# Kernel optimization log

Hardware: AMD Instinct MI355X
Metric: run time of the kernel (lower is better)

Reference implementation:

```python
import jax, jax.numpy as jnp
import numpy as np
from jax import lax

B, CIN, LIN = 65536, 1, 274
D, S, H, NL = 16, 18, 4, 4
DH = D // H  # 4
HID = 64
EPS = 1e-5

def layer_norm(x, g, b):
    m = jnp.mean(x, axis=-1, keepdims=True)
    v = jnp.mean(jnp.square(x - m), axis=-1, keepdims=True)
    return (x - m) * lax.rsqrt(v + EPS) * g + b

def setup_inputs() -> dict:
    key = jax.random.key(0)
    ks = jax.random.split(key, 16)
    n = lambda k, shp, s=0.05: jax.random.normal(k, shp, dtype=jnp.float32) * s
    return {
        "x": jax.random.normal(ks[0], (B, CIN, LIN), dtype=jnp.float32),
        "patch_w": n(ks[1], (D, CIN, 16), 0.2),   # Conv1d weight (O,I,K)
        "patch_b": jnp.zeros((D,), jnp.float32),
        "pos_embed": n(ks[2], (1, S, D), 0.02),
        "ln1_g": jnp.ones((NL, D), jnp.float32),
        "ln1_b": jnp.zeros((NL, D), jnp.float32),
        "qkv_w": n(ks[3], (NL, 3 * D, D), 0.2),    # in_proj_weight per layer
        "qkv_b": jnp.zeros((NL, 3 * D), jnp.float32),
        "out_w": n(ks[4], (NL, D, D), 0.2),
        "out_b": jnp.zeros((NL, D), jnp.float32),
        "ln2_g": jnp.ones((NL, D), jnp.float32),
        "ln2_b": jnp.zeros((NL, D), jnp.float32),
        "mlp_w1": n(ks[5], (NL, HID, D), 0.2),
        "mlp_b1": jnp.zeros((NL, HID), jnp.float32),
        "mlp_w2": n(ks[6], (NL, D, HID), 0.2),
        "mlp_b2": jnp.zeros((NL, D), jnp.float32),
        "lnf_g": jnp.ones((D,), jnp.float32),
        "lnf_b": jnp.zeros((D,), jnp.float32),
        "dec_w": n(ks[7], (D, CIN, 16), 0.2),      # ConvTranspose1d weight (I,O,K)
        "dec_b": jnp.zeros((CIN,), jnp.float32),
    }

def reference(x, patch_w, patch_b, pos_embed, ln1_g, ln1_b, qkv_w, qkv_b,
              out_w, out_b, ln2_g, ln2_b, mlp_w1, mlp_b1, mlp_w2, mlp_b2,
              lnf_g, lnf_b, dec_w, dec_b):
    dn = ('NCH', 'OIH', 'NCH')
    # patchify: (B,1,274) -> (B,16,18) -> (B,18,16)
    h = lax.conv_general_dilated(x, patch_w, (16,), [(7, 7)], dimension_numbers=dn)
    h = h + patch_b[None, :, None]
    h = jnp.transpose(h, (0, 2, 1)) + pos_embed
    scale = 1.0 / np.sqrt(DH)
    for i in range(NL):
        xn = layer_norm(h, ln1_g[i], ln1_b[i])
        qkv = xn @ qkv_w[i].T + qkv_b[i]                      # (B,S,3D)
        q, k, v = jnp.split(qkv, 3, axis=-1)
        q = q.reshape(B, S, H, DH)
        k = k.reshape(B, S, H, DH)
        v = v.reshape(B, S, H, DH)
        att = jnp.einsum('bqhd,bkhd->bhqk', q, k) * scale
        att = jax.nn.softmax(att, axis=-1)
        o = jnp.einsum('bhqk,bkhd->bqhd', att, v).reshape(B, S, D)
        h = h + (o @ out_w[i].T + out_b[i])
        xn2 = layer_norm(h, ln2_g[i], ln2_b[i])
        m = jax.nn.gelu(xn2 @ mlp_w1[i].T + mlp_b1[i], approximate=False)
        h = h + (m @ mlp_w2[i].T + mlp_b2[i])
    h = layer_norm(h, lnf_g, lnf_b)
    z = jnp.transpose(h, (0, 2, 1))                            # (B,16,18)
    # ConvTranspose1d(k=16, s=16, p=7): lhs_dilation=16, pad=k-1-p=8, flipped kernel
    w_t = jnp.transpose(jnp.flip(dec_w, axis=-1), (1, 0, 2))   # (O=1, I=16, 16)
    out = lax.conv_general_dilated(z, w_t, (1,), [(8, 8)], lhs_dilation=(16,),
                                   dimension_numbers=dn)
    out = out + dec_b[None, :, None]                            # (B,1,274)
    return out, z
```

## Files before the change

### kernel.cpp

```cpp
#include <hip/hip_runtime.h>
#include <math.h>
#include <stdint.h>

#define NB      65536
#define LIN     274
#define SEQ     18
#define DM      16
#define NH      4
#define HID     64
#define NLAYER  4
#define EPSF    1e-5f

#define EPB      8
#define NTHREADS 192
#define SMEM_F32 3456
#define VOFF_F32 1152

typedef _Float16 h2    __attribute__((ext_vector_type(2)));
typedef _Float16 f16x4 __attribute__((ext_vector_type(4)));
typedef float    f32x4 __attribute__((ext_vector_type(4)));
typedef __fp16   hf2_raw __attribute__((ext_vector_type(2)));

#if __has_builtin(__builtin_amdgcn_fdot2)
__device__ __forceinline__ float fdot2(h2 a, h2 b, float c) { return __builtin_amdgcn_fdot2(a, b, c, false); }
#else
__device__ __forceinline__ float fdot2(h2 a, h2 b, float c) { return c + (float)a[0] * (float)b[0] + (float)a[1] * (float)b[1]; }
#endif
#if __has_builtin(__builtin_amdgcn_cvt_pkrtz)
__device__ __forceinline__ h2 pkrtz(float a, float b) {
    hf2_raw r = __builtin_amdgcn_cvt_pkrtz(a, b);
    return __builtin_bit_cast(h2, r);
}
#else
__device__ __forceinline__ h2 pkrtz(float a, float b) { h2 r; r[0] = (_Float16)a; r[1] = (_Float16)b; return r; }
#endif

#if __has_builtin(__builtin_amdgcn_mfma_f32_16x16x16f16)
__device__ __forceinline__ f32x4 MFMA16(f16x4 a, f16x4 b, f32x4 c) {
    return __builtin_amdgcn_mfma_f32_16x16x16f16(a, b, c, 0, 0, 0);
}
#elif __has_builtin(__builtin_amdgcn_mfma_f32_16x16x16_f16)
__device__ __forceinline__ f32x4 MFMA16(f16x4 a, f16x4 b, f32x4 c) {
    return __builtin_amdgcn_mfma_f32_16x16x16_f16(a, b, c, 0, 0, 0);
}
#else
__device__ __forceinline__ f32x4 MFMA16(f16x4 a, f16x4 b, f32x4 c) {
    f32x4 d;
    asm volatile("v_mfma_f32_16x16x16_f16 %0, %1, %2, %3"
                 : "=v"(d) : "v"(a), "v"(b), "v"(c));
    return d;
}
#endif

__device__ __forceinline__ float fast_rcp(float x)  { return __builtin_amdgcn_rcpf(x); }
__device__ __forceinline__ float fast_rsq(float x)  { return __builtin_amdgcn_rsqf(x); }
__device__ __forceinline__ float fast_exp2(float x) { return __builtin_amdgcn_exp2f(x); }

__device__ __forceinline__ float gelu_tanh(float t) {
    const float A = 0.79788456080286536f;
    const float B = 0.03567740814183430f;
    float t2 = t * t;
    float u  = t * fmaf(t2, B, A);
    float e  = fast_exp2(u * 2.88539008177792681f);
    float r  = fast_rcp(e + 1.0f);
    return fmaf(-t, r, t);
}

__device__ __forceinline__ f16x4 pk4(float a, float b, float c, float d) {
    h2 lo = pkrtz(a, b), hi = pkrtz(c, d);
    f16x4 r; r[0] = lo[0]; r[1] = lo[1]; r[2] = hi[0]; r[3] = hi[1];
    return r;
}
__device__ __forceinline__ f32x4 ld4(const float* p) {
    float4 t = *(const float4*)p;
    f32x4 r; r[0] = t.x; r[1] = t.y; r[2] = t.z; r[3] = t.w;
    return r;
}

#define WS_H2_COUNT 6400

__global__ __launch_bounds__(512) void prep_weights(
    const float* __restrict__ patch_w, const float* __restrict__ dec_w,
    const float* __restrict__ qkv_w, const float* __restrict__ out_w,
    const float* __restrict__ mlp_w1, const float* __restrict__ mlp_w2,
    h2* __restrict__ ws)
{
    int i = blockIdx.x * 512 + threadIdx.x;
    if (i >= WS_H2_COUNT) return;
    int tile = i >> 7;
    int lane = (i >> 1) & 63;
    int p    = i & 1;
    int row  = lane & 15;
    int kb   = (lane >> 4) * 4 + 2 * p;
    float a, b;
    if (tile == 0)      { a = patch_w[row * 16 + kb];     b = patch_w[row * 16 + kb + 1]; }
    else if (tile == 1) { a = dec_w[kb * 16 + row];       b = dec_w[(kb + 1) * 16 + row]; }
    else {
        int t2 = tile - 2, li = t2 / 12, j = t2 % 12;
        const float* s;
        if (j < 3)       s = qkv_w  + li * 768  + (j * 16 + row) * 16 + kb;
        else if (j == 3) s = out_w  + li * 256  + row * 16 + kb;
        else if (j < 8)  s = mlp_w1 + li * 1024 + ((j - 4) * 16 + row) * 16 + kb;
        else             s = mlp_w2 + li * 1024 + row * 64 + (j - 8) * 16 + kb;
        a = s[0]; b = s[1];
    }
    ws[i] = pkrtz(a, b);
}

__global__ __launch_bounds__(NTHREADS) void ae_fwd(
    const float* __restrict__ x,
    const float* __restrict__ patch_b, const float* __restrict__ pos_embed,
    const float* __restrict__ ln1_g, const float* __restrict__ ln1_b,
    const h2*    __restrict__ wp,
    const float* __restrict__ qkv_b, const float* __restrict__ out_b,
    const float* __restrict__ ln2_g, const float* __restrict__ ln2_b,
    const float* __restrict__ mlp_b1, const float* __restrict__ mlp_b2,
    const float* __restrict__ lnf_g, const float* __restrict__ lnf_b,
    const float* __restrict__ dec_b,
    float* __restrict__ out_y, float* __restrict__ out_z)
{
    __shared__ float smem[SMEM_F32];
    const int tid  = threadIdx.x;
    const int lane = tid & 63;
    const int wv   = tid >> 6;
    const int col  = lane & 15;
    const int g16  = lane >> 4;
    const int fb   = g16 * 4;

    {
        const float4* xg = (const float4*)(x + (long long)blockIdx.x * (EPB * LIN));
        float4* xs = (float4*)smem;
        for (int i = tid; i < (EPB * LIN) / 4; i += NTHREADS) xs[i] = xg[i];
    }
    __syncthreads();

    int elemL[3], sIdx[3];
    #pragma unroll
    for (int t = 0; t < 3; ++t) {
        int T = wv * 48 + t * 16 + col;
        int e = (T * 57) >> 10;
        elemL[t] = e;
        sIdx[t]  = T - 18 * e;
    }

    const f16x4* wfrag = (const f16x4*)wp;
    const f16x4 wpatch = wfrag[lane];
    const f16x4 wdec   = wfrag[64 + lane];

    float hacc[3][4];
    {
        const float4 pb = *(const float4*)(patch_b + fb);
        #pragma unroll
        for (int t = 0; t < 3; ++t) {
            float xv[4];
            #pragma unroll
            for (int r = 0; r < 4; ++r) {
                int loc = sIdx[t] * 16 - 7 + fb + r;
                xv[r] = (loc >= 0 && loc < LIN) ? smem[elemL[t] * LIN + loc] : 0.0f;
            }
            f16x4 xb = pk4(xv[0], xv[1], xv[2], xv[3]);
            const float4 pe = *(const float4*)(pos_embed + sIdx[t] * DM + fb);
            f32x4 c; c[0] = pb.x + pe.x; c[1] = pb.y + pe.y; c[2] = pb.z + pe.z; c[3] = pb.w + pe.w;
            c = MFMA16(wpatch, xb, c);
            #pragma unroll
            for (int r = 0; r < 4; ++r) hacc[t][r] = c[r];
        }
    }

    h2*    Kl = (h2*)smem;
    float* Vl = smem + VOFF_F32;

    #pragma unroll 1
    for (int li = 0; li < NLAYER; ++li) {
        const f16x4* wl = wfrag + (2 + li * 12) * 64 + lane;

        const float4 g1 = *(const float4*)(ln1_g + li * DM + fb);
        const float4 b1 = *(const float4*)(ln1_b + li * DM + fb);
        h2 qp[3][2]; f16x4 kpk[3]; f32x4 vreg[3];
        #pragma unroll
        for (int t = 0; t < 3; ++t) {
            float a0 = hacc[t][0], a1 = hacc[t][1], a2 = hacc[t][2], a3 = hacc[t][3];
            float sm = a0 + a1 + a2 + a3;
            sm += __shfl_xor(sm, 16); sm += __shfl_xor(sm, 32);
            float mean = sm * (1.0f / 16.0f);
            float d0 = a0 - mean, d1 = a1 - mean, d2 = a2 - mean, d3 = a3 - mean;
            float vs = d0 * d0 + d1 * d1 + d2 * d2 + d3 * d3;
            vs += __shfl_xor(vs, 16); vs += __shfl_xor(vs, 32);
            float inv = fast_rsq(vs * (1.0f / 16.0f) + EPSF);
            f16x4 xb = pk4(d0 * inv * g1.x + b1.x, d1 * inv * g1.y + b1.y,
                           d2 * inv * g1.z + b1.z, d3 * inv * g1.w + b1.w);
            f32x4 aq = ld4(qkv_b + li * 48 + fb);
            f32x4 ak = ld4(qkv_b + li * 48 + 16 + fb);
            f32x4 av = ld4(qkv_b + li * 48 + 32 + fb);
            aq = MFMA16(wl[0],   xb, aq);
            ak = MFMA16(wl[64],  xb, ak);
            av = MFMA16(wl[128], xb, av);
            const float qs = 0.72134752044448170f;
            qp[t][0] = pkrtz(aq[0] * qs, aq[1] * qs);
            qp[t][1] = pkrtz(aq[2] * qs, aq[3] * qs);
            kpk[t] = pk4(ak[0], ak[1], ak[2], ak[3]);
            vreg[t] = av;
        }
        __syncthreads();
        #pragma unroll
        for (int t = 0; t < 3; ++t) {
            ((f16x4*)Kl)[elemL[t] * 72 + g16 * 18 + sIdx[t]] = kpk[t];
            float4 vv; vv.x = vreg[t][0]; vv.y = vreg[t][1]; vv.z = vreg[t][2]; vv.w = vreg[t][3];
            *(float4*)(Vl + elemL[t] * 288 + (g16 * 18 + sIdx[t]) * 4) = vv;
        }
        __syncthreads();

        const float4 ob4 = *(const float4*)(out_b + li * DM + fb);
        #pragma unroll
        for (int t = 0; t < 3; ++t) {
            const f16x4* kb = (const f16x4*)Kl + elemL[t] * 72 + g16 * 18;
            float sc[SEQ]; float ssum = 0.0f;
            #pragma unroll
            for (int j = 0; j < SEQ; ++j) {
                f16x4 kj = kb[j];
                h2 k0; k0[0] = kj[0]; k0[1] = kj[1];
                h2 k1; k1[0] = kj[2]; k1[1] = kj[3];
                float sv = fdot2(qp[t][1], k1, fdot2(qp[t][0], k0, 0.0f));
                float w  = fast_exp2(sv);
                sc[j] = w; ssum += w;
            }
            float inv = fast_rcp(ssum);
            const float4* vb = (const float4*)(Vl + elemL[t] * 288 + g16 * 72);
            float o0 = 0.f, o1 = 0.f, o2 = 0.f, o3 = 0.f;
            #pragma unroll
            for (int j = 0; j < SEQ; ++j) {
                float4 vj = vb[j];
                float w = sc[j];
                o0 = fmaf(w, vj.x, o0); o1 = fmaf(w, vj.y, o1);
                o2 = fmaf(w, vj.z, o2); o3 = fmaf(w, vj.w, o3);
            }
            f16x4 obf = pk4(o0 * inv, o1 * inv, o2 * inv, o3 * inv);
            f32x4 oa; oa[0] = ob4.x; oa[1] = ob4.y; oa[2] = ob4.z; oa[3] = ob4.w;
            oa = MFMA16(wl[3 * 64], obf, oa);
            #pragma unroll
            for (int r = 0; r < 4; ++r) hacc[t][r] += oa[r];
        }

        const float4 g2 = *(const float4*)(ln2_g + li * DM + fb);
        const float4 b2 = *(const float4*)(ln2_b + li * DM + fb);
        #pragma unroll
        for (int t = 0; t < 3; ++t) {
            float a0 = hacc[t][0], a1 = hacc[t][1], a2 = hacc[t][2], a3 = hacc[t][3];
            float sm = a0 + a1 + a2 + a3;
            sm += __shfl_xor(sm, 16); sm += __shfl_xor(sm, 32);
            float mean = sm * (1.0f / 16.0f);
            float d0 = a0 - mean, d1 = a1 - mean, d2 = a2 - mean, d3 = a3 - mean;
            float vs = d0 * d0 + d1 * d1 + d2 * d2 + d3 * d3;
            vs += __shfl_xor(vs, 16); vs += __shfl_xor(vs, 32);
            float inv = fast_rsq(vs * (1.0f / 16.0f) + EPSF);
            f16x4 xb2 = pk4(d0 * inv * g2.x + b2.x, d1 * inv * g2.y + b2.y,
                            d2 * inv * g2.z + b2.z, d3 * inv * g2.w + b2.w);
            f32x4 acc2 = ld4(mlp_b2 + li * DM + fb);
            #pragma unroll
            for (int c = 0; c < 4; ++c) {
                f32x4 m1 = ld4(mlp_b1 + li * HID + c * 16 + fb);
                m1 = MFMA16(wl[(4 + c) * 64], xb2, m1);
                f16x4 gb = pk4(gelu_tanh(m1[0]), gelu_tanh(m1[1]),
                               gelu_tanh(m1[2]), gelu_tanh(m1[3]));
                acc2 = MFMA16(wl[(8 + c) * 64], gb, acc2);
            }
            #pragma unroll
            for (int r = 0; r < 4; ++r) hacc[t][r] += acc2[r];
        }
    }

    const float4 gf = *(const float4*)(lnf_g + fb);
    const float4 bf = *(const float4*)(lnf_b + fb);
    const float db0 = dec_b[0];
    #pragma unroll
    for (int t = 0; t < 3; ++t) {
        float a0 = hacc[t][0], a1 = hacc[t][1], a2 = hacc[t][2], a3 = hacc[t][3];
        float sm = a0 + a1 + a2 + a3;
        sm += __shfl_xor(sm, 16); sm += __shfl_xor(sm, 32);
        float mean = sm * (1.0f / 16.0f);
        float d0 = a0 - mean, d1 = a1 - mean, d2 = a2 - mean, d3 = a3 - mean;
        float vs = d0 * d0 + d1 * d1 + d2 * d2 + d3 * d3;
        vs += __shfl_xor(vs, 16); vs += __shfl_xor(vs, 32);
        float inv = fast_rsq(vs * (1.0f / 16.0f) + EPSF);
        float f0 = d0 * inv * gf.x + bf.x;
        float f1 = d1 * inv * gf.y + bf.y;
        float f2 = d2 * inv * gf.z + bf.z;
        float f3 = d3 * inv * gf.w + bf.w;

        long long eg = (long long)blockIdx.x * EPB + elemL[t];
        float* zb = out_z + eg * (DM * SEQ) + sIdx[t];
        zb[(fb + 0) * SEQ] = f0; zb[(fb + 1) * SEQ] = f1;
        zb[(fb + 2) * SEQ] = f2; zb[(fb + 3) * SEQ] = f3;

        f16x4 hb = pk4(f0, f1, f2, f3);
        f32x4 y4 = {0.f, 0.f, 0.f, 0.f};
        y4 = MFMA16(wdec, hb, y4);
        float* yb = out_y + eg * LIN;
        int p0 = sIdx[t] * 16 + fb - 7;
        #pragma unroll
        for (int r = 0; r < 4; ++r) {
            int p = p0 + r;
            if (p >= 0 && p < LIN) yb[p] = y4[r] + db0;
        }
    }
}

#define EPB_F 14
#define NT_F  252
__global__ __launch_bounds__(NT_F) void ae_fwd_f32(
    const float* __restrict__ x,
    const float* __restrict__ patch_w, const float* __restrict__ patch_b,
    const float* __restrict__ pos_embed,
    const float* __restrict__ ln1_g, const float* __restrict__ ln1_b,
    const float* __restrict__ qkv_w, const float* __restrict__ qkv_b,
    const float* __restrict__ out_w, const float* __restrict__ out_b,
    const float* __restrict__ ln2_g, const float* __restrict__ ln2_b,
    const float* __restrict__ mlp_w1, const float* __restrict__ mlp_b1,
    const float* __restrict__ mlp_w2, const float* __restrict__ mlp_b2,
    const float* __restrict__ lnf_g, const float* __restrict__ lnf_b,
    const float* __restrict__ dec_w, const float* __restrict__ dec_b,
    float* __restrict__ out_y, float* __restrict__ out_z)
{
    __shared__ float s_kv[EPB_F * 580];
    const int tid = threadIdx.x;
    const int e   = tid / SEQ;
    const int s   = tid - e * SEQ;
    const long long b = (long long)blockIdx.x * EPB_F + e;
    const bool valid = (b < NB);
    {
        const long long base = (long long)blockIdx.x * (EPB_F * LIN);
        const long long lim  = (long long)NB * LIN - 1;
        for (int i = tid; i < EPB_F * LIN; i += NT_F) {
            long long gi = base + i;
            if (gi > lim) gi = lim;
            s_kv[i] = x[gi];
        }
    }
    __syncthreads();
    float xv[16];
    {
        const float* xe = &s_kv[e * LIN];
        #pragma unroll
        for (int k = 0; k < 16; ++k) {
            int idx = s * 16 - 7 + k;
            xv[k] = (idx >= 0 && idx < LIN) ? xe[idx] : 0.0f;
        }
    }
    float h[DM];
    #pragma unroll
    for (int d = 0; d < DM; ++d) {
        float acc = patch_b[d] + pos_embed[s * DM + d];
        #pragma unroll
        for (int k = 0; k < 16; ++k) acc = fmaf(xv[k], patch_w[d * 16 + k], acc);
        h[d] = acc;
    }
    #pragma unroll 1
    for (int li = 0; li < NLAYER; ++li) {
        float xn[DM];
        {
            float m = 0.f;
            #pragma unroll
            for (int d = 0; d < DM; ++d) m += h[d];
            m *= (1.0f / DM);
            float v = 0.f;
            #pragma unroll
            for (int d = 0; d < DM; ++d) { float t = h[d] - m; v = fmaf(t, t, v); }
            v *= (1.0f / DM);
            float inv = fast_rsq(v + EPSF);
            #pragma unroll
            for (int d = 0; d < DM; ++d) xn[d] = (h[d] - m) * inv * ln1_g[li * DM + d] + ln1_b[li * DM + d];
        }
        float q[DM], kk[DM], vv[DM];
        {
            const float* W  = qkv_w + li * 48 * DM;
            const float* Wb = qkv_b + li * 48;
            #pragma unroll
            for (int j = 0; j < DM; ++j) {
                float aq = Wb[j], ak = Wb[DM + j], av = Wb[2 * DM + j];
                #pragma unroll
                for (int d = 0; d < DM; ++d) {
                    float xd = xn[d];
                    aq = fmaf(xd, W[j * DM + d], aq);
                    ak = fmaf(xd, W[(DM + j) * DM + d], ak);
                    av = fmaf(xd, W[(2 * DM + j) * DM + d], av);
                }
                q[j] = aq; kk[j] = ak; vv[j] = av;
            }
        }
        __syncthreads();
        {
            float* kb = &s_kv[e * 580];
            float* vb = kb + SEQ * DM;
            #pragma unroll
            for (int j = 0; j < DM; ++j) kb[s * DM + j] = kk[j];
            #pragma unroll
            for (int j = 0; j < DM; ++j) vb[s * DM + j] = vv[j];
        }
        __syncthreads();
        float o[DM];
        {
            const float* kb = &s_kv[e * 580];
            const float* vb = kb + SEQ * DM;
            #pragma unroll
            for (int hh = 0; hh < NH; ++hh) {
                const float qscale = 0.5f * 1.44269504088896341f;
                const float q0 = q[hh * 4] * qscale, q1 = q[hh * 4 + 1] * qscale;
                const float q2 = q[hh * 4 + 2] * qscale, q3 = q[hh * 4 + 3] * qscale;
                float sc[SEQ];
                float ssum = 0.f;
                #pragma unroll
                for (int j = 0; j < SEQ; ++j) {
                    const float4 kj = *(const float4*)(kb + j * DM + hh * 4);
                    float t = fmaf(q0, kj.x, fmaf(q1, kj.y, fmaf(q2, kj.z, q3 * kj.w)));
                    float w = fast_exp2(t);
                    sc[j] = w; ssum += w;
                }
                const float inv = fast_rcp(ssum);
                float a0 = 0.f, a1 = 0.f, a2 = 0.f, a3 = 0.f;
                #pragma unroll
                for (int j = 0; j < SEQ; ++j) {
                    const float4 vj = *(const float4*)(vb + j * DM + hh * 4);
                    const float w = sc[j] * inv;
                    a0 = fmaf(w, vj.x, a0); a1 = fmaf(w, vj.y, a1);
                    a2 = fmaf(w, vj.z, a2); a3 = fmaf(w, vj.w, a3);
                }
                o[hh * 4] = a0; o[hh * 4 + 1] = a1; o[hh * 4 + 2] = a2; o[hh * 4 + 3] = a3;
            }
        }
        {
            const float* W  = out_w + li * DM * DM;
            #pragma unroll
            for (int d = 0; d < DM; ++d) {
                float acc = out_b[li * DM + d];
                #pragma unroll
                for (int d2 = 0; d2 < DM; ++d2) acc = fmaf(o[d2], W[d * DM + d2], acc);
                h[d] += acc;
            }
        }
        float xn2[DM];
        {
            float m = 0.f;
            #pragma unroll
            for (int d = 0; d < DM; ++d) m += h[d];
            m *= (1.0f / DM);
            float v = 0.f;
            #pragma unroll
            for (int d = 0; d < DM; ++d) { float t = h[d] - m; v = fmaf(t, t, v); }
            v *= (1.0f / DM);
            float inv = fast_rsq(v + EPSF);
            #pragma unroll
            for (int d = 0; d < DM; ++d) xn2[d] = (h[d] - m) * inv * ln2_g[li * DM + d] + ln2_b[li * DM + d];
        }
        {
            const float* W1 = mlp_w1 + li * HID * DM;
            const float* W2 = mlp_w2 + li * DM * HID;
            float acc2[DM];
            #pragma unroll
            for (int d = 0; d < DM; ++d) acc2[d] = mlp_b2[li * DM + d];
            #pragma unroll 2
            for (int j = 0; j < HID; ++j) {
                float t = mlp_b1[li * HID + j];
                #pragma unroll
                for (int d = 0; d < DM; ++d) t = fmaf(xn2[d], W1[j * DM + d], t);
                float g = gelu_tanh(t);
                #pragma unroll
                for (int d = 0; d < DM; ++d) acc2[d] = fmaf(g, W2[d * HID + j], acc2[d]);
            }
            #pragma unroll
            for (int d = 0; d < DM; ++d) h[d] += acc2[d];
        }
    }
    {
        float m = 0.f;
        #pragma unroll
        for (int d = 0; d < DM; ++d) m += h[d];
        m *= (1.0f / DM);
        float v = 0.f;
        #pragma unroll
        for (int d = 0; d < DM; ++d) { float t = h[d] - m; v = fmaf(t, t, v); }
        v *= (1.0f / DM);
        float inv = fast_rsq(v + EPSF);
        #pragma unroll
        for (int d = 0; d < DM; ++d) h[d] = (h[d] - m) * inv * lnf_g[d] + lnf_b[d];
    }
    if (valid) {
        float* zb = out_z + b * (DM * SEQ);
        #pragma unroll
        for (int d = 0; d < DM; ++d) zb[d * SEQ + s] = h[d];
        float* yb = out_y + b * LIN;
        const float db0 = dec_b[0];
        #pragma unroll
        for (int k = 0; k < 16; ++k) {
            int t = s * 16 + k - 7;
            if (t >= 0 && t < LIN) {
                float acc = db0;
                #pragma unroll
                for (int d = 0; d < DM; ++d) acc = fmaf(h[d], dec_w[d * 16 + k], acc);
                yb[t] = acc;
            }
        }
    }
}

extern "C" void kernel_launch(void* const* d_in, const int* in_sizes, int n_in,
                              void* d_out, int out_size, void* d_ws, size_t ws_size,
                              hipStream_t stream) {
    const float* x        = (const float*)d_in[0];
    const float* patch_w  = (const float*)d_in[1];
    const float* patch_b  = (const float*)d_in[2];
    const float* pos_e    = (const float*)d_in[3];
    const float* ln1_g    = (const float*)d_in[4];
    const float* ln1_b    = (const float*)d_in[5];
    const float* qkv_w    = (const float*)d_in[6];
    const float* qkv_b    = (const float*)d_in[7];
    const float* out_w    = (const float*)d_in[8];
    const float* out_b    = (const float*)d_in[9];
    const float* ln2_g    = (const float*)d_in[10];
    const float* ln2_b    = (const float*)d_in[11];
    const float* mlp_w1   = (const float*)d_in[12];
    const float* mlp_b1   = (const float*)d_in[13];
    const float* mlp_w2   = (const float*)d_in[14];
    const float* mlp_b2   = (const float*)d_in[15];
    const float* lnf_g    = (const float*)d_in[16];
    const float* lnf_b    = (const float*)d_in[17];
    const float* dec_w    = (const float*)d_in[18];
    const float* dec_b    = (const float*)d_in[19];

    float* out_y = (float*)d_out;
    float* out_z = out_y + (long long)NB * LIN;

    if (ws_size >= WS_H2_COUNT * sizeof(h2)) {
        h2* wsp = (h2*)d_ws;
        prep_weights<<<(WS_H2_COUNT + 511) / 512, 512, 0, stream>>>(
            patch_w, dec_w, qkv_w, out_w, mlp_w1, mlp_w2, wsp);
        ae_fwd<<<NB / EPB, NTHREADS, 0, stream>>>(
            x, patch_b, pos_e, ln1_g, ln1_b, wsp,
            qkv_b, out_b, ln2_g, ln2_b, mlp_b1, mlp_b2,
            lnf_g, lnf_b, dec_b, out_y, out_z);
    } else {
        const int grid = (NB + EPB_F - 1) / EPB_F;
        ae_fwd_f32<<<grid, NT_F, 0, stream>>>(
            x, patch_w, patch_b, pos_e, ln1_g, ln1_b, qkv_w, qkv_b,
            out_w, out_b, ln2_g, ln2_b, mlp_w1, mlp_b1, mlp_w2, mlp_b2,
            lnf_g, lnf_b, dec_w, dec_b, out_y, out_z);
    }
}
```

Baseline: 475.6 us.

## Fold LayerNorm affine and query scale into weights, use fp16 transposed V attention

The prep kernel now folds the LN1/LN2 gains into the QKV and MLP1 weight fragments, folds the LN biases and the query scale into precomputed biases, and writes those biases to the workspace. LayerNorm in the main kernel becomes a single-pass mean/sum-of-squares with fma normalisation. V is stored in shared memory as transposed fp16 and K is read with 16-byte loads, so attention uses packed fp16 softmax weights and fdot2 for both the sum and the PV product. This removes per-element ALU work and halves V shared-memory traffic, at the cost of fp16 softmax weights and a one-pass variance that is less numerically robust.

Measured after the change: 490.7 us. +3.2%, slower.

```diff
diff --git a/kernel.cpp b/kernel.cpp
--- a/kernel.cpp
+++ b/kernel.cpp
@@ -13,11 +13,14 @@
 
 #define EPB      8
 #define NTHREADS 192
-#define SMEM_F32 3456
-#define VOFF_F32 1152
+#define SMEM_F32 2688
+#define VT_BYTE_OFF 4608
+
+#define QS 0.72134752044448170f
 
 typedef _Float16 h2    __attribute__((ext_vector_type(2)));
 typedef _Float16 f16x4 __attribute__((ext_vector_type(4)));
+typedef _Float16 f16x8 __attribute__((ext_vector_type(8)));
 typedef float    f32x4 __attribute__((ext_vector_type(4)));
 typedef __fp16   hf2_raw __attribute__((ext_vector_type(2)));
 
@@ -57,11 +60,10 @@
 __device__ __forceinline__ float fast_exp2(float x) { return __builtin_amdgcn_exp2f(x); }
 
 __device__ __forceinline__ float gelu_tanh(float t) {
-    const float A = 0.79788456080286536f;
-    const float B = 0.03567740814183430f;
-    float t2 = t * t;
-    float u  = t * fmaf(t2, B, A);
-    float e  = fast_exp2(u * 2.88539008177792681f);
+    const float A2 = 0.79788456080286536f * 2.88539008177792681f;
+    const float B2 = 0.03567740814183430f * 2.88539008177792681f;
+    float u  = t * fmaf(t * t, B2, A2);
+    float e  = fast_exp2(u);
     float r  = fast_rcp(e + 1.0f);
     return fmaf(-t, r, t);
 }
@@ -76,45 +78,81 @@
     f32x4 r; r[0] = t.x; r[1] = t.y; r[2] = t.z; r[3] = t.w;
     return r;
 }
+__device__ __forceinline__ h2 h2at(f16x8 v, int i) {
+    h2 r; r[0] = v[2 * i]; r[1] = v[2 * i + 1]; return r;
+}
 
 #define WS_H2_COUNT 6400
+#define WS_BIAS_FLOATS (NLAYER * 112)
+#define WS_TOTAL_BYTES (WS_H2_COUNT * 4 + WS_BIAS_FLOATS * 4)
+#define PREP_ITEMS (WS_H2_COUNT + WS_BIAS_FLOATS)
 
 __global__ __launch_bounds__(512) void prep_weights(
     const float* __restrict__ patch_w, const float* __restrict__ dec_w,
     const float* __restrict__ qkv_w, const float* __restrict__ out_w,
     const float* __restrict__ mlp_w1, const float* __restrict__ mlp_w2,
+    const float* __restrict__ ln1_g, const float* __restrict__ ln1_b,
+    const float* __restrict__ ln2_g, const float* __restrict__ ln2_b,
+    const float* __restrict__ qkv_b, const float* __restrict__ mlp_b1,
     h2* __restrict__ ws)
 {
     int i = blockIdx.x * 512 + threadIdx.x;
-    if (i >= WS_H2_COUNT) return;
-    int tile = i >> 7;
-    int lane = (i >> 1) & 63;
-    int p    = i & 1;
-    int row  = lane & 15;
-    int kb   = (lane >> 4) * 4 + 2 * p;
-    float a, b;
-    if (tile == 0)      { a = patch_w[row * 16 + kb];     b = patch_w[row * 16 + kb + 1]; }
-    else if (tile == 1) { a = dec_w[kb * 16 + row];       b = dec_w[(kb + 1) * 16 + row]; }
-    else {
-        int t2 = tile - 2, li = t2 / 12, j = t2 % 12;
-        const float* s;
-        if (j < 3)       s = qkv_w  + li * 768  + (j * 16 + row) * 16 + kb;
-        else if (j == 3) s = out_w  + li * 256  + row * 16 + kb;
-        else if (j < 8)  s = mlp_w1 + li * 1024 + ((j - 4) * 16 + row) * 16 + kb;
-        else             s = mlp_w2 + li * 1024 + row * 64 + (j - 8) * 16 + kb;
-        a = s[0]; b = s[1];
-    }
-    ws[i] = pkrtz(a, b);
+    if (i >= PREP_ITEMS) return;
+    if (i < WS_H2_COUNT) {
+        int tile = i >> 7;
+        int lane = (i >> 1) & 63;
+        int p    = i & 1;
+        int row  = lane & 15;
+        int kb   = (lane >> 4) * 4 + 2 * p;
+        float a, b;
+        if (tile == 0)      { a = patch_w[row * 16 + kb];  b = patch_w[row * 16 + kb + 1]; }
+        else if (tile == 1) { a = dec_w[kb * 16 + row];    b = dec_w[(kb + 1) * 16 + row]; }
+        else {
+            int t2 = tile - 2, li = t2 / 12, j = t2 % 12;
+            const float* s;
+            float g0 = 1.0f, g1v = 1.0f;
+            if (j < 3) {
+                s = qkv_w + li * 768 + (j * 16 + row) * 16 + kb;
+                g0 = ln1_g[li * 16 + kb]; g1v = ln1_g[li * 16 + kb + 1];
+                if (j == 0) { g0 *= QS; g1v *= QS; }
+            } else if (j == 3) {
+                s = out_w + li * 256 + row * 16 + kb;
+            } else if (j < 8) {
+                s = mlp_w1 + li * 1024 + ((j - 4) * 16 + row) * 16 + kb;
+                g0 = ln2_g[li * 16 + kb]; g1v = ln2_g[li * 16 + kb + 1];
+            } else {
+                s = mlp_w2 + li * 1024 + row * 64 + (j - 8) * 16 + kb;
+            }
+            a = s[0] * g0; b = s[1] * g1v;
+        }
+        ws[i] = pkrtz(a, b);
+    } else {
+        int t = i - WS_H2_COUNT;
+        int li = t / 112, r = t % 112;
+        float* wbf = (float*)(ws + WS_H2_COUNT);
+        float bv;
+        if (r < 48) {
+            const float* Wr = qkv_w + li * 768 + r * 16;
+            const float* lb = ln1_b + li * 16;
+            bv = qkv_b[li * 48 + r];
+            for (int d = 0; d < 16; ++d) bv = fmaf(Wr[d], lb[d], bv);
+            if (r < 16) bv *= QS;
+        } else {
+            int j = r - 48;
+            const float* Wr = mlp_w1 + li * 1024 + j * 16;
+            const float* lb = ln2_b + li * 16;
+            bv = mlp_b1[li * 64 + j];
+            for (int d = 0; d < 16; ++d) bv = fmaf(Wr[d], lb[d], bv);
+        }
+        wbf[li * 112 + r] = bv;
+    }
 }
 
 __global__ __launch_bounds__(NTHREADS) void ae_fwd(
     const float* __restrict__ x,
     const float* __restrict__ patch_b, const float* __restrict__ pos_embed,
-    const float* __restrict__ ln1_g, const float* __restrict__ ln1_b,
-    const h2*    __restrict__ wp,
-    const float* __restrict__ qkv_b, const float* __restrict__ out_b,
-    const float* __restrict__ ln2_g, const float* __restrict__ ln2_b,
-    const float* __restrict__ mlp_b1, const float* __restrict__ mlp_b2,
+    const h2*    __restrict__ wp, const float* __restrict__ wb,
+    const float* __restrict__ out_b, const float* __restrict__ mlp_b2,
     const float* __restrict__ lnf_g, const float* __restrict__ lnf_b,
     const float* __restrict__ dec_b,
     float* __restrict__ out_y, float* __restrict__ out_z)
@@ -146,6 +184,7 @@
     const f16x4* wfrag = (const f16x4*)wp;
     const f16x4 wpatch = wfrag[lane];
     const f16x4 wdec   = wfrag[64 + lane];
+    h2 ones2; ones2[0] = (_Float16)1.0f; ones2[1] = (_Float16)1.0f;
 
     float hacc[3][4];
     {
@@ -167,99 +206,111 @@
         }
     }
 
-    h2*    Kl = (h2*)smem;
-    float* Vl = smem + VOFF_F32;
-
     #pragma unroll 1
     for (int li = 0; li < NLAYER; ++li) {
         const f16x4* wl = wfrag + (2 + li * 12) * 64 + lane;
-
-        const float4 g1 = *(const float4*)(ln1_g + li * DM + fb);
-        const float4 b1 = *(const float4*)(ln1_b + li * DM + fb);
-        h2 qp[3][2]; f16x4 kpk[3]; f32x4 vreg[3];
+        const float* wbL = wb + li * 112;
+        const f32x4 bq = ld4(wbL + fb);
+        const f32x4 bk = ld4(wbL + 16 + fb);
+        const f32x4 bv = ld4(wbL + 32 + fb);
+        f32x4 b1r[4];
+        #pragma unroll
+        for (int c = 0; c < 4; ++c) b1r[c] = ld4(wbL + 48 + c * 16 + fb);
+        const float4 ob4 = *(const float4*)(out_b + li * DM + fb);
+        const f32x4 b2r = ld4(mlp_b2 + li * DM + fb);
+
+        h2 qp[3][2]; f16x4 kpk[3], vpk[3];
         #pragma unroll
         for (int t = 0; t < 3; ++t) {
             float a0 = hacc[t][0], a1 = hacc[t][1], a2 = hacc[t][2], a3 = hacc[t][3];
             float sm = a0 + a1 + a2 + a3;
+            float qq = fmaf(a0, a0, fmaf(a1, a1, fmaf(a2, a2, a3 * a3)));
             sm += __shfl_xor(sm, 16); sm += __shfl_xor(sm, 32);
+            qq += __shfl_xor(qq, 16); qq += __shfl_xor(qq, 32);
             float mean = sm * (1.0f / 16.0f);
-            float d0 = a0 - mean, d1 = a1 - mean, d2 = a2 - mean, d3 = a3 - mean;
-            float vs = d0 * d0 + d1 * d1 + d2 * d2 + d3 * d3;
-            vs += __shfl_xor(vs, 16); vs += __shfl_xor(vs, 32);
-            float inv = fast_rsq(vs * (1.0f / 16.0f) + EPSF);
-            f16x4 xb = pk4(d0 * inv * g1.x + b1.x, d1 * inv * g1.y + b1.y,
-                           d2 * inv * g1.z + b1.z, d3 * inv * g1.w + b1.w);
-            f32x4 aq = ld4(qkv_b + li * 48 + fb);
-            f32x4 ak = ld4(qkv_b + li * 48 + 16 + fb);
-            f32x4 av = ld4(qkv_b + li * 48 + 32 + fb);
-            aq = MFMA16(wl[0],   xb, aq);
-            ak = MFMA16(wl[64],  xb, ak);
-            av = MFMA16(wl[128], xb, av);
-            const float qs = 0.72134752044448170f;
-            qp[t][0] = pkrtz(aq[0] * qs, aq[1] * qs);
-            qp[t][1] = pkrtz(aq[2] * qs, aq[3] * qs);
+            float var  = fmaxf(fmaf(mean, -mean, qq * (1.0f / 16.0f)), 0.0f);
+            float inv  = fast_rsq(var + EPSF);
+            float mi   = mean * inv;
+            f16x4 xb = pk4(fmaf(a0, inv, -mi), fmaf(a1, inv, -mi),
+                           fmaf(a2, inv, -mi), fmaf(a3, inv, -mi));
+            f32x4 aq = MFMA16(wl[0],   xb, bq);
+            f32x4 ak = MFMA16(wl[64],  xb, bk);
+            f32x4 av = MFMA16(wl[128], xb, bv);
+            qp[t][0] = pkrtz(aq[0], aq[1]);
+            qp[t][1] = pkrtz(aq[2], aq[3]);
             kpk[t] = pk4(ak[0], ak[1], ak[2], ak[3]);
-            vreg[t] = av;
+            vpk[t] = pk4(av[0], av[1], av[2], av[3]);
         }
         __syncthreads();
         #pragma unroll
         for (int t = 0; t < 3; ++t) {
-            ((f16x4*)Kl)[elemL[t] * 72 + g16 * 18 + sIdx[t]] = kpk[t];
-            float4 vv; vv.x = vreg[t][0]; vv.y = vreg[t][1]; vv.z = vreg[t][2]; vv.w = vreg[t][3];
-            *(float4*)(Vl + elemL[t] * 288 + (g16 * 18 + sIdx[t]) * 4) = vv;
+            ((f16x4*)smem)[(elemL[t] * 4 + g16) * 18 + sIdx[t]] = kpk[t];
+            _Float16* vt = (_Float16*)((char*)smem + VT_BYTE_OFF) + elemL[t] * 384 + g16 * 24 + sIdx[t];
+            vt[0]   = vpk[t][0];
+            vt[96]  = vpk[t][1];
+            vt[192] = vpk[t][2];
+            vt[288] = vpk[t][3];
         }
         __syncthreads();
 
-        const float4 ob4 = *(const float4*)(out_b + li * DM + fb);
         #pragma unroll
         for (int t = 0; t < 3; ++t) {
-            const f16x4* kb = (const f16x4*)Kl + elemL[t] * 72 + g16 * 18;
-            float sc[SEQ]; float ssum = 0.0f;
-            #pragma unroll
-            for (int j = 0; j < SEQ; ++j) {
-                f16x4 kj = kb[j];
-                h2 k0; k0[0] = kj[0]; k0[1] = kj[1];
-                h2 k1; k1[0] = kj[2]; k1[1] = kj[3];
-                float sv = fdot2(qp[t][1], k1, fdot2(qp[t][0], k0, 0.0f));
-                float w  = fast_exp2(sv);
-                sc[j] = w; ssum += w;
-            }
-            float inv = fast_rcp(ssum);
-            const float4* vb = (const float4*)(Vl + elemL[t] * 288 + g16 * 72);
-            float o0 = 0.f, o1 = 0.f, o2 = 0.f, o3 = 0.f;
-            #pragma unroll
-            for (int j = 0; j < SEQ; ++j) {
-                float4 vj = vb[j];
-                float w = sc[j];
-                o0 = fmaf(w, vj.x, o0); o1 = fmaf(w, vj.y, o1);
-                o2 = fmaf(w, vj.z, o2); o3 = fmaf(w, vj.w, o3);
-            }
-            f16x4 obf = pk4(o0 * inv, o1 * inv, o2 * inv, o3 * inv);
+            const char* Kb = (const char*)smem + (elemL[t] * 4 + g16) * 144;
+            const char* Vb = (const char*)smem + VT_BYTE_OFF + elemL[t] * 768 + g16 * 48;
+            h2 w9[9];
+            #pragma unroll
+            for (int jp = 0; jp < 9; ++jp) {
+                f16x8 k2 = *(const f16x8*)(Kb + jp * 16);
+                float s0 = fdot2(qp[t][1], h2at(k2, 1), fdot2(qp[t][0], h2at(k2, 0), 0.0f));
+                float s1 = fdot2(qp[t][1], h2at(k2, 3), fdot2(qp[t][0], h2at(k2, 2), 0.0f));
+                w9[jp] = pkrtz(fast_exp2(s0), fast_exp2(s1));
+            }
+            float sA = 0.0f, sB = 0.0f;
+            #pragma unroll
+            for (int jp = 0; jp < 8; jp += 2) {
+                sA = fdot2(w9[jp], ones2, sA);
+                sB = fdot2(w9[jp + 1], ones2, sB);
+            }
+            sA = fdot2(w9[8], ones2, sA);
+            float inv = fast_rcp(sA + sB);
+            float o[4];
+            #pragma unroll
+            for (int d = 0; d < 4; ++d) {
+                const char* vr = Vb + d * 192;
+                f16x8 v8a = *(const f16x8*)vr;
+                f16x8 v8b = *(const f16x8*)(vr + 16);
+                h2 vtl = *(const h2*)(vr + 32);
+                float acc = fdot2(w9[8], vtl, 0.0f);
+                #pragma unroll
+                for (int jp = 0; jp < 4; ++jp) acc = fdot2(w9[jp], h2at(v8a, jp), acc);
+                #pragma unroll
+                for (int jp = 0; jp < 4; ++jp) acc = fdot2(w9[4 + jp], h2at(v8b, jp), acc);
+                o[d] = acc * inv;
+            }
+            f16x4 obf = pk4(o[0], o[1], o[2], o[3]);
             f32x4 oa; oa[0] = ob4.x; oa[1] = ob4.y; oa[2] = ob4.z; oa[3] = ob4.w;
-            oa = MFMA16(wl[3 * 64], obf, oa);
+            oa = MFMA16(wl[192], obf, oa);
             #pragma unroll
             for (int r = 0; r < 4; ++r) hacc[t][r] += oa[r];
         }
 
-        const float4 g2 = *(const float4*)(ln2_g + li * DM + fb);
-        const float4 b2 = *(const float4*)(ln2_b + li * DM + fb);
         #pragma unroll
         for (int t = 0; t < 3; ++t) {
             float a0 = hacc[t][0], a1 = hacc[t][1], a2 = hacc[t][2], a3 = hacc[t][3];
             float sm = a0 + a1 + a2 + a3;
+            float qq = fmaf(a0, a0, fmaf(a1, a1, fmaf(a2, a2, a3 * a3)));
             sm += __shfl_xor(sm, 16); sm += __shfl_xor(sm, 32);
+            qq += __shfl_xor(qq, 16); qq += __shfl_xor(qq, 32);
             float mean = sm * (1.0f / 16.0f);
-            float d0 = a0 - mean, d1 = a1 - mean, d2 = a2 - mean, d3 = a3 - mean;
-            float vs = d0 * d0 + d1 * d1 + d2 * d2 + d3 * d3;
-            vs += __shfl_xor(vs, 16); vs += __shfl_xor(vs, 32);
-            float inv = fast_rsq(vs * (1.0f / 16.0f) + EPSF);
-            f16x4 xb2 = pk4(d0 * inv * g2.x + b2.x, d1 * inv * g2.y + b2.y,
-                            d2 * inv * g2.z + b2.z, d3 * inv * g2.w + b2.w);
-            f32x4 acc2 = ld4(mlp_b2 + li * DM + fb);
+            float var  = fmaxf(fmaf(mean, -mean, qq * (1.0f / 16.0f)), 0.0f);
+            float inv  = fast_rsq(var + EPSF);
+            float mi   = mean * inv;
+            f16x4 xb2 = pk4(fmaf(a0, inv, -mi), fmaf(a1, inv, -mi),
+                            fmaf(a2, inv, -mi), fmaf(a3, inv, -mi));
+            f32x4 acc2 = b2r;
             #pragma unroll
             for (int c = 0; c < 4; ++c) {
-                f32x4 m1 = ld4(mlp_b1 + li * HID + c * 16 + fb);
-                m1 = MFMA16(wl[(4 + c) * 64], xb2, m1);
+                f32x4 m1 = MFMA16(wl[(4 + c) * 64], xb2, b1r[c]);
                 f16x4 gb = pk4(gelu_tanh(m1[0]), gelu_tanh(m1[1]),
                                gelu_tanh(m1[2]), gelu_tanh(m1[3]));
                 acc2 = MFMA16(wl[(8 + c) * 64], gb, acc2);
@@ -276,16 +327,17 @@
     for (int t = 0; t < 3; ++t) {
         float a0 = hacc[t][0], a1 = hacc[t][1], a2 = hacc[t][2], a3 = hacc[t][3];
         float sm = a0 + a1 + a2 + a3;
+        float qq = fmaf(a0, a0, fmaf(a1, a1, fmaf(a2, a2, a3 * a3)));
         sm += __shfl_xor(sm, 16); sm += __shfl_xor(sm, 32);
+        qq += __shfl_xor(qq, 16); qq += __shfl_xor(qq, 32);
         float mean = sm * (1.0f / 16.0f);
-        float d0 = a0 - mean, d1 = a1 - mean, d2 = a2 - mean, d3 = a3 - mean;
-        float vs = d0 * d0 + d1 * d1 + d2 * d2 + d3 * d3;
-        vs += __shfl_xor(vs, 16); vs += __shfl_xor(vs, 32);
-        float inv = fast_rsq(vs * (1.0f / 16.0f) + EPSF);
-        float f0 = d0 * inv * gf.x + bf.x;
-        float f1 = d1 * inv * gf.y + bf.y;
-        float f2 = d2 * inv * gf.z + bf.z;
-        float f3 = d3 * inv * gf.w + bf.w;
+        float var  = fmaxf(fmaf(mean, -mean, qq * (1.0f / 16.0f)), 0.0f);
+        float inv  = fast_rsq(var + EPSF);
+        float mi   = mean * inv;
+        float f0 = fmaf(fmaf(a0, inv, -mi), gf.x, bf.x);
+        float f1 = fmaf(fmaf(a1, inv, -mi), gf.y, bf.y);
+        float f2 = fmaf(fmaf(a2, inv, -mi), gf.z, bf.z);
+        float f3 = fmaf(fmaf(a3, inv, -mi), gf.w, bf.w);
 
         long long eg = (long long)blockIdx.x * EPB + elemL[t];
         float* zb = out_z + eg * (DM * SEQ) + sIdx[t];
@@ -529,14 +581,15 @@
     float* out_y = (float*)d_out;
     float* out_z = out_y + (long long)NB * LIN;
 
-    if (ws_size >= WS_H2_COUNT * sizeof(h2)) {
+    if (ws_size >= WS_TOTAL_BYTES) {
         h2* wsp = (h2*)d_ws;
-        prep_weights<<<(WS_H2_COUNT + 511) / 512, 512, 0, stream>>>(
-            patch_w, dec_w, qkv_w, out_w, mlp_w1, mlp_w2, wsp);
+        const float* wbp = (const float*)(wsp + WS_H2_COUNT);
+        prep_weights<<<(PREP_ITEMS + 511) / 512, 512, 0, stream>>>(
+            patch_w, dec_w, qkv_w, out_w, mlp_w1, mlp_w2,
+            ln1_g, ln1_b, ln2_g, ln2_b, qkv_b, mlp_b1, wsp);
         ae_fwd<<<NB / EPB, NTHREADS, 0, stream>>>(
-            x, patch_b, pos_e, ln1_g, ln1_b, wsp,
-            qkv_b, out_b, ln2_g, ln2_b, mlp_b1, mlp_b2,
-            lnf_g, lnf_b, dec_b, out_y, out_z);
+            x, patch_b, pos_e, wsp, wbp,
+            out_b, mlp_b2, lnf_g, lnf_b, dec_b, out_y, out_z);
     } else {
         const int grid = (NB + EPB_F - 1) / EPB_F;
         ae_fwd_f32<<<grid, NT_F, 0, stream>>>(
```
